# Kernel optimization log

Measured on AMD Instinct MI355X. Metric: run time of the kernel, lower is better.

## Reference

```python
import jax, jax.numpy as jnp
import numpy as np
from jax import lax

BITS = 8
CLIP = 2.0 ** (BITS - 1) - 1.0  # 127 for int8 symmetric quantization
EPS = 1e-6


def _quantize(x):
    """Dynamic per-tensor symmetric quantization (AQT-style).

    Returns the integer-valued (but float-dtype) quantized tensor and the
    scale such that dequant = q / scale.
    """
    bound = jnp.maximum(jnp.max(jnp.abs(x)), EPS)
    scale = CLIP / bound
    q = jnp.clip(jnp.round(x * scale), -CLIP, CLIP)
    return q, scale


def setup_inputs() -> dict:
    key = jax.random.key(0)
    k1, k2 = jax.random.split(key)
    lhs = jax.random.normal(k1, (4096, 4096), dtype=jnp.float32)
    rhs = jax.random.normal(k2, (4096, 4096), dtype=jnp.float32)
    return {"lhs": lhs, "rhs": rhs}


def reference(lhs, rhs):
    # Quantize both operands with dynamically computed per-tensor scales,
    # do the matmul on the integer-valued tensors, then dequantize the
    # result by the product of scales. This is the math aqt_ops.aqt_dot
    q_lhs, s_lhs = _quantize(lhs)
    q_rhs, s_rhs = _quantize(rhs)
    acc = jnp.matmul(q_lhs, q_rhs)  # [M, N], integer-valued accumulation
    return acc / (s_lhs * s_rhs)
```

## Files before the change

### kernel.cpp

```cpp
#include <hip/hip_runtime.h>
#include <hip/hip_bf16.h>


typedef int v4i __attribute__((ext_vector_type(4)));
typedef int v16i __attribute__((ext_vector_type(16)));

#define MAT_N 4096

__device__ __forceinline__ void async_copy16(const void* g, void* l) {
    __builtin_amdgcn_global_load_lds(
        (const __attribute__((address_space(1))) void*)g,
        (__attribute__((address_space(3))) void*)l,
        16, 0, 0);
}

__device__ __forceinline__ unsigned uabs_bits(float f) {
    return __float_as_uint(f) & 0x7fffffffu;
}

__global__ __launch_bounds__(256) void absmax_partial_kernel(
    const float4* __restrict__ lhs, const float4* __restrict__ rhs,
    unsigned* __restrict__ pmax) {
    const int b = blockIdx.x;
    const float4* x = (b < 512) ? lhs : rhs;
    const float4* p = x + (size_t)(b & 511) * 8192;
    unsigned m0 = 0, m1 = 0, m2 = 0, m3 = 0;
#pragma unroll 8
    for (int u = 0; u < 32; u++) {
        float4 v = p[u * 256 + threadIdx.x];
        m0 = max(m0, uabs_bits(v.x));
        m1 = max(m1, uabs_bits(v.y));
        m2 = max(m2, uabs_bits(v.z));
        m3 = max(m3, uabs_bits(v.w));
    }
    unsigned m = max(max(m0, m1), max(m2, m3));
#pragma unroll
    for (int off = 32; off > 0; off >>= 1)
        m = max(m, (unsigned)__shfl_down(m, off, 64));
    __shared__ unsigned sm[4];
    if ((threadIdx.x & 63) == 0) sm[threadIdx.x >> 6] = m;
    __syncthreads();
    if (threadIdx.x == 0)
        pmax[b] = max(max(sm[0], sm[1]), max(sm[2], sm[3]));
}

__global__ __launch_bounds__(256) void quant_fused_kernel(
    const float* __restrict__ lhs, const float* __restrict__ rhs,
    unsigned char* __restrict__ qA, signed char* __restrict__ qBT,
    const unsigned* __restrict__ pmax) {
    const int N = MAT_N;
    const int t = threadIdx.x;
    int b = blockIdx.x;
    __shared__ __align__(16) signed char smT[64 * 80];
    __shared__ unsigned red[4];
    __shared__ float s_sh;

    const int slot0 = (b < 4096) ? 0 : 512;
    unsigned mm = max(pmax[slot0 + t], pmax[slot0 + 256 + t]);
#pragma unroll
    for (int off = 32; off > 0; off >>= 1)
        mm = max(mm, (unsigned)__shfl_down(mm, off, 64));
    if ((t & 63) == 0) red[t >> 6] = mm;
    __syncthreads();
    if (t == 0) {
        unsigned f = max(max(red[0], red[1]), max(red[2], red[3]));
        s_sh = 127.0f / fmaxf(__uint_as_float(f), 1e-6f);
    }
    __syncthreads();
    const float s = s_sh;

    if (b < 4096) {
        const float4* x4 = (const float4*)lhs;
        unsigned* q4 = (unsigned*)qA;
        const int base4 = b * 1024;
#pragma unroll
        for (int u = 0; u < 4; u++) {
            int idx = base4 + u * 256 + t;
            float4 v = x4[idx];
            int a = min(127, max(-127, (int)rintf(v.x * s)));
            int bq = min(127, max(-127, (int)rintf(v.y * s)));
            int c = min(127, max(-127, (int)rintf(v.z * s)));
            int d = min(127, max(-127, (int)rintf(v.w * s)));
            q4[idx] = (unsigned)(a & 0xff) | ((unsigned)(bq & 0xff) << 8) |
                      ((unsigned)(c & 0xff) << 16) | ((unsigned)(d & 0xff) << 24);
        }
    } else {
        b -= 4096;
        const int n0 = (b & 63) * 64;
        const int k0 = (b >> 6) * 64;
        const int mk = t >> 4;
        const int mn = t & 15;
        const float4* x4 = (const float4*)rhs;

        unsigned w[4];
#pragma unroll
        for (int i = 0; i < 4; i++) {
            float4 v = x4[(size_t)(k0 + 4 * mk + i) * (N / 4) + (n0 >> 2) + mn];
            int a = min(127, max(-127, (int)rintf(v.x * s)));
            int bq = min(127, max(-127, (int)rintf(v.y * s)));
            int c = min(127, max(-127, (int)rintf(v.z * s)));
            int d = min(127, max(-127, (int)rintf(v.w * s)));
            w[i] = (unsigned)(a & 0xff) | ((unsigned)(bq & 0xff) << 8) |
                   ((unsigned)(c & 0xff) << 16) | ((unsigned)(d & 0xff) << 24);
        }
#pragma unroll
        for (int j = 0; j < 4; j++) {
            unsigned selj = (unsigned)j | ((unsigned)(4 + j) << 8) |
                            ((unsigned)j << 16) | ((unsigned)(4 + j) << 24);
            unsigned p01 = __builtin_amdgcn_perm(w[1], w[0], selj);
            unsigned p23 = __builtin_amdgcn_perm(w[3], w[2], selj);
            unsigned uj = __builtin_amdgcn_perm(p23, p01, 0x05040100u);
            *(unsigned*)(smT + (4 * mn + j) * 80 + 4 * mk) = uj;
        }
        __syncthreads();
        const int nr = t >> 2;
        const int kq = (t & 3) * 16;
        int4 val = *(const int4*)(smT + nr * 80 + kq);
        *(int4*)(qBT + (size_t)(n0 + nr) * N + k0 + kq) = val;
    }
}

__global__ __launch_bounds__(256) void gemm_i8_kernel(
    const signed char* __restrict__ A, const signed char* __restrict__ BT,
    float* __restrict__ C, const unsigned* __restrict__ pmax) {
    const int N = MAT_N;
    __shared__ __align__(16) signed char As[128 * 128];
    __shared__ __align__(16) signed char Bs[128 * 128];

    const int tid = threadIdx.x;
    const int wave = tid >> 6;
    const int lane = tid & 63;
    const int m32 = lane & 31;
    const int h = lane >> 5;
    const int wr = (wave >> 1) * 64;
    const int wc = (wave & 1) * 64;

    const int flat = blockIdx.x;
    const int super = flat >> 6;
    const int within = flat & 63;
    const int bx = (super & 3) * 8 + (within & 7);
    const int by = (super >> 2) * 8 + (within >> 3);
    const int brow = by * 128;
    const int bcol = bx * 128;

    v16i acc[2][2] = {};

    int gaoff[4], gboff[4];
    signed char* la[4];
    signed char* lb[4];
#pragma unroll
    for (int u = 0; u < 4; u++) {
        int c = tid + 256 * u;
        int r = c >> 3;
        int q = (c & 7) ^ ((r ^ (r >> 3)) & 7);
        gaoff[u] = (brow + r) * N + q * 16;
        gboff[u] = (bcol + r) * N + q * 16;
        la[u] = As + c * 16;
        lb[u] = Bs + c * 16;
    }

    int abase[2], avr[2], bbase[2], bvr[2];
#pragma unroll
    for (int i = 0; i < 2; i++) {
        int r = wr + i * 32 + m32;
        abase[i] = r * 8;
        avr[i] = (r ^ (r >> 3)) & 7;
        r = wc + i * 32 + m32;
        bbase[i] = r * 8;
        bvr[i] = (r ^ (r >> 3)) & 7;
    }

    for (int k0 = 0; k0 < N; k0 += 128) {
        __syncthreads();
#pragma unroll
        for (int u = 0; u < 4; u++) async_copy16(A + gaoff[u] + k0, la[u]);
#pragma unroll
        for (int u = 0; u < 4; u++) async_copy16(BT + gboff[u] + k0, lb[u]);
        __syncthreads();

#pragma unroll
        for (int s = 0; s < 4; s++) {
            const int q = 2 * s + h;
            v4i af[2], bf[2];
#pragma unroll
            for (int i = 0; i < 2; i++)
                af[i] = *(const v4i*)(As + (abase[i] + (q ^ avr[i])) * 16);
#pragma unroll
            for (int j = 0; j < 2; j++)
                bf[j] = *(const v4i*)(Bs + (bbase[j] + (q ^ bvr[j])) * 16);
#pragma unroll
            for (int i = 0; i < 2; i++)
#pragma unroll
                for (int j = 0; j < 2; j++)
                    acc[i][j] = __builtin_amdgcn_mfma_i32_32x32x32_i8(
                        af[i], bf[j], acc[i][j], 0, 0, 0);
        }
    }

    __shared__ unsigned redl[4], redr[4];
    unsigned ml = max(pmax[tid], pmax[tid + 256]);
    unsigned mr = max(pmax[512 + tid], pmax[768 + tid]);
#pragma unroll
    for (int off = 32; off > 0; off >>= 1) {
        ml = max(ml, (unsigned)__shfl_down(ml, off, 64));
        mr = max(mr, (unsigned)__shfl_down(mr, off, 64));
    }
    if (lane == 0) { redl[wave] = ml; redr[wave] = mr; }
    __syncthreads();
    const float bl = fmaxf(
        __uint_as_float(max(max(redl[0], redl[1]), max(redl[2], redl[3]))), 1e-6f);
    const float br = fmaxf(
        __uint_as_float(max(max(redr[0], redr[1]), max(redr[2], redr[3]))), 1e-6f);
    const float dq = bl * br * (1.0f / (127.0f * 127.0f));

#pragma unroll
    for (int i = 0; i < 2; i++)
#pragma unroll
        for (int j = 0; j < 2; j++) {
            const int col = bcol + wc + j * 32 + m32;
#pragma unroll
            for (int reg = 0; reg < 16; reg++) {
                const int row =
                    brow + wr + i * 32 + (reg & 3) + 8 * (reg >> 2) + 4 * h;
                C[(size_t)row * N + col] = (float)acc[i][j][reg] * dq;
            }
        }
}

extern "C" void kernel_launch(void* const* d_in, const int* in_sizes, int n_in,
                              void* d_out, int out_size, void* d_ws, size_t ws_size,
                              hipStream_t stream) {
    const float* lhs = (const float*)d_in[0];
    const float* rhs = (const float*)d_in[1];
    float* out = (float*)d_out;

    unsigned* pmax = (unsigned*)d_ws;
    signed char* qA = (signed char*)d_ws + 8192;
    signed char* qBT = qA + (size_t)MAT_N * MAT_N;

    absmax_partial_kernel<<<1024, 256, 0, stream>>>(
        (const float4*)lhs, (const float4*)rhs, pmax);
    quant_fused_kernel<<<8192, 256, 0, stream>>>(
        lhs, rhs, (unsigned char*)qA, qBT, pmax);
    gemm_i8_kernel<<<1024, 256, 0, stream>>>(qA, qBT, out, pmax);
}
```

Measured before the change: 258.9 us.

## Enlarge GEMM tile to 256x256 with double-buffered LDS and XCD-aware mapping

The int8 GEMM moves from 128x128 tiles with 4 waves to 256x256 tiles with 8 waves. Each wave now computes 4x2 MFMA tiles, and global-to-LDS loads are double-buffered with explicit vmcnt waits and barriers, so loads overlap with compute. Blocks are mapped to XCDs for L2 locality, and s_setprio is raised around the MFMA bursts. Using 128KB of LDS and many accumulator registers limits occupancy to one block per CU, and only 256 blocks are launched, which may underfill the GPU.

Result: no change. 256.2 us (-1.0%).

```diff
diff --git a/kernel.cpp b/kernel.cpp
--- a/kernel.cpp
+++ b/kernel.cpp
@@ -120,86 +120,128 @@
     }
 }
 
-__global__ __launch_bounds__(256) void gemm_i8_kernel(
+__global__ __launch_bounds__(512, 2) void gemm_i8_kernel(
     const signed char* __restrict__ A, const signed char* __restrict__ BT,
     float* __restrict__ C, const unsigned* __restrict__ pmax) {
     const int N = MAT_N;
-    __shared__ __align__(16) signed char As[128 * 128];
-    __shared__ __align__(16) signed char Bs[128 * 128];
+    __shared__ __align__(16) signed char As[2][256 * 128];
+    __shared__ __align__(16) signed char Bs[2][256 * 128];
+    __shared__ unsigned redl[8], redr[8];
 
     const int tid = threadIdx.x;
     const int wave = tid >> 6;
     const int lane = tid & 63;
     const int m32 = lane & 31;
     const int h = lane >> 5;
-    const int wr = (wave >> 1) * 64;
-    const int wc = (wave & 1) * 64;
-
-    const int flat = blockIdx.x;
-    const int super = flat >> 6;
-    const int within = flat & 63;
-    const int bx = (super & 3) * 8 + (within & 7);
-    const int by = (super >> 2) * 8 + (within >> 3);
-    const int brow = by * 128;
-    const int bcol = bx * 128;
-
-    v16i acc[2][2] = {};
-
-    int gaoff[4], gboff[4];
-    signed char* la[4];
-    signed char* lb[4];
+    const int wm = wave >> 2;
+    const int wn = wave & 3;
+
+    const int bid = blockIdx.x;
+    const int xcd = bid & 7;
+    const int bi = bid >> 3;
+    const int by = (xcd >> 1) * 4 + (bi >> 3);
+    const int bx = (xcd & 1) * 8 + (bi & 7);
+    const int brow = by * 256;
+    const int bcol = bx * 256;
+
+    v16i acc[4][2] = {};
+
+    int gaoff[4], gboff[4], lofs[4];
 #pragma unroll
     for (int u = 0; u < 4; u++) {
-        int c = tid + 256 * u;
+        int c = tid + 512 * u;
         int r = c >> 3;
         int q = (c & 7) ^ ((r ^ (r >> 3)) & 7);
         gaoff[u] = (brow + r) * N + q * 16;
         gboff[u] = (bcol + r) * N + q * 16;
-        la[u] = As + c * 16;
-        lb[u] = Bs + c * 16;
-    }
-
-    int abase[2], avr[2], bbase[2], bvr[2];
-#pragma unroll
-    for (int i = 0; i < 2; i++) {
-        int r = wr + i * 32 + m32;
-        abase[i] = r * 8;
-        avr[i] = (r ^ (r >> 3)) & 7;
-        r = wc + i * 32 + m32;
-        bbase[i] = r * 8;
-        bvr[i] = (r ^ (r >> 3)) & 7;
-    }
-
-    for (int k0 = 0; k0 < N; k0 += 128) {
-        __syncthreads();
-#pragma unroll
-        for (int u = 0; u < 4; u++) async_copy16(A + gaoff[u] + k0, la[u]);
-#pragma unroll
-        for (int u = 0; u < 4; u++) async_copy16(BT + gboff[u] + k0, lb[u]);
-        __syncthreads();
-
-#pragma unroll
-        for (int s = 0; s < 4; s++) {
-            const int q = 2 * s + h;
-            v4i af[2], bf[2];
-#pragma unroll
-            for (int i = 0; i < 2; i++)
-                af[i] = *(const v4i*)(As + (abase[i] + (q ^ avr[i])) * 16);
-#pragma unroll
-            for (int j = 0; j < 2; j++)
-                bf[j] = *(const v4i*)(Bs + (bbase[j] + (q ^ bvr[j])) * 16);
-#pragma unroll
-            for (int i = 0; i < 2; i++)
-#pragma unroll
-                for (int j = 0; j < 2; j++)
-                    acc[i][j] = __builtin_amdgcn_mfma_i32_32x32x32_i8(
-                        af[i], bf[j], acc[i][j], 0, 0, 0);
-        }
-    }
-
-    __shared__ unsigned redl[4], redr[4];
-    unsigned ml = max(pmax[tid], pmax[tid + 256]);
-    unsigned mr = max(pmax[512 + tid], pmax[768 + tid]);
+        lofs[u] = c * 16;
+    }
+
+    int arow[4], av[4];
+#pragma unroll
+    for (int mi = 0; mi < 4; mi++) {
+        int r = wm * 128 + mi * 32 + m32;
+        arow[mi] = r * 128;
+        av[mi] = (r ^ (r >> 3)) & 7;
+    }
+    int bro[2], bv[2];
+#pragma unroll
+    for (int nj = 0; nj < 2; nj++) {
+        int r = wn * 64 + nj * 32 + m32;
+        bro[nj] = r * 128;
+        bv[nj] = (r ^ (r >> 3)) & 7;
+    }
+
+    auto stage = [&](int buf, int koff) {
+#pragma unroll
+        for (int u = 0; u < 4; u++)
+            async_copy16(A + gaoff[u] + koff, &As[buf][lofs[u]]);
+#pragma unroll
+        for (int u = 0; u < 4; u++)
+            async_copy16(BT + gboff[u] + koff, &Bs[buf][lofs[u]]);
+    };
+
+    auto slice = [&](const signed char* as_, const signed char* bs_, int s) {
+        v4i af[4], bf[2];
+        const int q = 2 * s + h;
+#pragma unroll
+        for (int mi = 0; mi < 4; mi++)
+            af[mi] = *(const v4i*)(as_ + arow[mi] + ((q ^ av[mi]) << 4));
+#pragma unroll
+        for (int nj = 0; nj < 2; nj++)
+            bf[nj] = *(const v4i*)(bs_ + bro[nj] + ((q ^ bv[nj]) << 4));
+        __builtin_amdgcn_s_setprio(1);
+#pragma unroll
+        for (int mi = 0; mi < 4; mi++)
+#pragma unroll
+            for (int nj = 0; nj < 2; nj++)
+                acc[mi][nj] = __builtin_amdgcn_mfma_i32_32x32x32_i8(
+                    af[mi], bf[nj], acc[mi][nj], 0, 0, 0);
+        __builtin_amdgcn_s_setprio(0);
+    };
+
+    stage(0, 0);
+    stage(1, 128);
+    asm volatile("s_waitcnt vmcnt(8)" ::: "memory");
+    __builtin_amdgcn_s_barrier();
+    __builtin_amdgcn_sched_barrier(0);
+
+    for (int t = 0; t < 30; ++t) {
+        const signed char* as_ = As[t & 1];
+        const signed char* bs_ = Bs[t & 1];
+        slice(as_, bs_, 0);
+        slice(as_, bs_, 1);
+        slice(as_, bs_, 2);
+        slice(as_, bs_, 3);
+        __builtin_amdgcn_s_barrier();
+        __builtin_amdgcn_sched_barrier(0);
+        stage(t & 1, (t + 2) * 128);
+        asm volatile("s_waitcnt vmcnt(8)" ::: "memory");
+        __builtin_amdgcn_s_barrier();
+        __builtin_amdgcn_sched_barrier(0);
+    }
+    {
+        const signed char* as_ = As[0];
+        const signed char* bs_ = Bs[0];
+        slice(as_, bs_, 0);
+        slice(as_, bs_, 1);
+        slice(as_, bs_, 2);
+        slice(as_, bs_, 3);
+        asm volatile("s_waitcnt vmcnt(0)" ::: "memory");
+        __builtin_amdgcn_s_barrier();
+        __builtin_amdgcn_sched_barrier(0);
+    }
+    {
+        const signed char* as_ = As[1];
+        const signed char* bs_ = Bs[1];
+        slice(as_, bs_, 0);
+        slice(as_, bs_, 1);
+        slice(as_, bs_, 2);
+        slice(as_, bs_, 3);
+    }
+
+    unsigned ml = pmax[tid];
+    unsigned mr = pmax[512 + tid];
 #pragma unroll
     for (int off = 32; off > 0; off >>= 1) {
         ml = max(ml, (unsigned)__shfl_down(ml, off, 64));
@@ -207,22 +249,26 @@
     }
     if (lane == 0) { redl[wave] = ml; redr[wave] = mr; }
     __syncthreads();
-    const float bl = fmaxf(
-        __uint_as_float(max(max(redl[0], redl[1]), max(redl[2], redl[3]))), 1e-6f);
-    const float br = fmaxf(
-        __uint_as_float(max(max(redr[0], redr[1]), max(redr[2], redr[3]))), 1e-6f);
+    unsigned fl = redl[0], fr = redr[0];
+#pragma unroll
+    for (int k = 1; k < 8; k++) {
+        fl = max(fl, redl[k]);
+        fr = max(fr, redr[k]);
+    }
+    const float bl = fmaxf(__uint_as_float(fl), 1e-6f);
+    const float br = fmaxf(__uint_as_float(fr), 1e-6f);
     const float dq = bl * br * (1.0f / (127.0f * 127.0f));
 
 #pragma unroll
-    for (int i = 0; i < 2; i++)
-#pragma unroll
-        for (int j = 0; j < 2; j++) {
-            const int col = bcol + wc + j * 32 + m32;
+    for (int mi = 0; mi < 4; mi++)
+#pragma unroll
+        for (int nj = 0; nj < 2; nj++) {
+            const int col = bcol + wn * 64 + nj * 32 + m32;
 #pragma unroll
             for (int reg = 0; reg < 16; reg++) {
                 const int row =
-                    brow + wr + i * 32 + (reg & 3) + 8 * (reg >> 2) + 4 * h;
-                C[(size_t)row * N + col] = (float)acc[i][j][reg] * dq;
+                    brow + wm * 128 + mi * 32 + (reg & 3) + 8 * (reg >> 2) + 4 * h;
+                C[(size_t)row * N + col] = (float)acc[mi][nj][reg] * dq;
             }
         }
 }
@@ -242,5 +288,5 @@
         (const float4*)lhs, (const float4*)rhs, pmax);
     quant_fused_kernel<<<8192, 256, 0, stream>>>(
         lhs, rhs, (unsigned char*)qA, qBT, pmax);
-    gemm_i8_kernel<<<1024, 256, 0, stream>>>(qA, qBT, out, pmax);
-}
+    gemm_i8_kernel<<<256, 512, 0, stream>>>(qA, qBT, out, pmax);
+}
```
